# Kernel tuning notes

Measured on AMD Instinct MI355X. Metric: run time of the kernel, lower is better.

## Reference

```python
import jax, jax.numpy as jnp
import numpy as np

WIN = 7
N_HEADS = 12


def _swin_rel_pos_index(win_h, win_w):
    # standard Swin relative position index, flattened to (win_h*win_w)**2
    coords = np.stack(np.meshgrid(np.arange(win_h), np.arange(win_w), indexing='ij'))  # 2, Wh, Ww
    coords_flat = coords.reshape(2, -1)
    rel = coords_flat[:, :, None] - coords_flat[:, None, :]  # 2, N, N
    rel = rel.transpose(1, 2, 0).astype(np.int64)
    rel[:, :, 0] += win_h - 1
    rel[:, :, 1] += win_w - 1
    rel[:, :, 0] *= 2 * win_w - 1
    return rel.sum(-1).reshape(-1).astype(np.int32)  # (N*N,)


def setup_inputs() -> dict:
    key = jax.random.key(0)
    ks = jax.random.split(key, 8)
    B_, N, C = 4096, WIN * WIN, 384
    num_win = 64
    x = jax.random.normal(ks[0], (B_, N, C), dtype=jnp.float32)
    # 0 / -inf style additive mask (use -100 like Swin's masked_fill value)
    m = jax.random.uniform(ks[1], (num_win, N, N))
    mask = jnp.where(m < 0.5, 0.0, -100.0).astype(jnp.float32)
    qkv_w = jax.random.normal(ks[2], (3 * C, C), dtype=jnp.float32) * 0.02
    qkv_b = jax.random.normal(ks[3], (3 * C,), dtype=jnp.float32) * 0.02
    proj_w = jax.random.normal(ks[4], (C, C), dtype=jnp.float32) * 0.02
    proj_b = jax.random.normal(ks[5], (C,), dtype=jnp.float32) * 0.02
    bias_table = jax.random.normal(ks[6], ((2 * WIN - 1) ** 2, N_HEADS), dtype=jnp.float32) * 0.02
    rel_index = jnp.asarray(_swin_rel_pos_index(WIN, WIN))
    return {"x": x, "mask": mask, "qkv_w": qkv_w, "qkv_b": qkv_b,
            "proj_w": proj_w, "proj_b": proj_b, "bias_table": bias_table,
            "rel_index": rel_index}


def reference(x, mask, qkv_w, qkv_b, proj_w, proj_b, bias_table, rel_index):
    B_, N, C = x.shape
    H = N_HEADS
    hd = C // H
    scale = hd ** (-0.5)
    # qkv projection: (B_, N, 3C) -> (3, B_, H, N, hd)
    qkv = (jnp.einsum('bnc,oc->bno', x, qkv_w) + qkv_b)
    qkv = qkv.reshape(B_, N, 3, H, hd).transpose(2, 0, 3, 1, 4)
    q, k, v = qkv[0] * scale, qkv[1], qkv[2]
    attn = jnp.einsum('bhnd,bhmd->bhnm', q, k)  # (B_, H, N, N)
    # relative position bias gather: (N*N, H) -> (H, N, N)
    bias = bias_table[rel_index].reshape(N, N, H).transpose(2, 0, 1)
    attn = attn + bias[None]
    num_win = mask.shape[0]
    attn = attn.reshape(B_ // num_win, num_win, H, N, N) + mask[None, :, None]
    attn = attn.reshape(B_, H, N, N)
    attn = jax.nn.softmax(attn, axis=-1)
    out = jnp.einsum('bhnm,bhmd->bnhd', attn, v).reshape(B_, N, H * hd)
    out = jnp.einsum('bnc,oc->bno', out, proj_w) + proj_b
    return out
```

## Files before the change

### kernel.cpp

```cpp
#include <hip/hip_runtime.h>
#include <hip/hip_bf16.h>
#include <stdint.h>
#include <stddef.h>


typedef __attribute__((ext_vector_type(8))) __bf16 bf16x8;
typedef __attribute__((ext_vector_type(4))) float f32x4;
typedef __attribute__((ext_vector_type(4))) unsigned short u16x4;

typedef const unsigned int __attribute__((address_space(1)))* gptr_t;
typedef unsigned int __attribute__((address_space(3)))* lptr_t;

#define SCALE 0.17677669529663687f

__device__ __forceinline__ unsigned short f2bf(float f) {
  union { float f; unsigned int u; } c; c.f = f;
  unsigned int r = c.u + 0x7fffu + ((c.u >> 16) & 1u);
  return (unsigned short)(r >> 16);
}

__device__ __forceinline__ void gl_lds16(const void* g, void* s) {
  __builtin_amdgcn_global_load_lds((gptr_t)g, (lptr_t)s, 16, 0, 0);
}

__global__ __launch_bounds__(256) void convert_kernel(
    const float* __restrict__ x, unsigned short* __restrict__ xb, long nx4,
    const float* __restrict__ w1, unsigned short* __restrict__ w1b, long n14,
    const float* __restrict__ w2, unsigned short* __restrict__ w2b, long n24) {
  long stride = (long)gridDim.x * blockDim.x;
  long t0 = (long)blockIdx.x * blockDim.x + threadIdx.x;
  for (long i = t0; i < nx4; i += stride) {
    f32x4 v = ((const f32x4*)x)[i];
    u16x4 o;
#pragma unroll
    for (int j = 0; j < 4; ++j) o[j] = f2bf(v[j]);
    ((u16x4*)xb)[i] = o;
  }
  for (long i = t0; i < n14; i += stride) {
    f32x4 v = ((const f32x4*)w1)[i];
    u16x4 o;
#pragma unroll
    for (int j = 0; j < 4; ++j) o[j] = f2bf(v[j]);
    ((u16x4*)w1b)[i] = o;
  }
  for (long i = t0; i < n24; i += stride) {
    f32x4 v = ((const f32x4*)w2)[i];
    u16x4 o;
#pragma unroll
    for (int j = 0; j < 4; ++j) o[j] = f2bf(v[j]);
    ((u16x4*)w2b)[i] = o;
  }
}

__global__ __launch_bounds__(256) void cmb_kernel(
    const float* __restrict__ mask, const float* __restrict__ bias_table,
    const int* __restrict__ rel_index, float* __restrict__ cmb) {
  int idx = blockIdx.x * 256 + threadIdx.x;
  int j = idx & 63, i = (idx >> 6) & 63;
  int hw = idx >> 12;
  int h = hw % 12, w = hw / 12;
  float v = -1e30f;
  if (i < 49 && j < 49)
    v = bias_table[rel_index[i * 49 + j] * 12 + h] + mask[(w * 49 + i) * 49 + j];
  cmb[idx] = v;
}

template <int NBN, int KDIM, bool OUT_BF16>
__global__ __launch_bounds__(256) void gemm_nt(
    const unsigned short* __restrict__ A, const unsigned short* __restrict__ Bw,
    const float* __restrict__ bias, unsigned short* __restrict__ Cb,
    float* __restrict__ Cf, int Nn) {
  __shared__ __align__(16) unsigned short As[128 * 32];
  __shared__ __align__(16) unsigned short Bs[128 * 32];
  const int tid = threadIdx.x;
  const int w = tid >> 6, l = tid & 63, q = l >> 4, ln = l & 15;
  const int bm = blockIdx.x / NBN, bn = blockIdx.x % NBN;
  const unsigned short* Ab = A + (size_t)bm * 128 * KDIM;
  const unsigned short* Bb = Bw + (size_t)bn * 128 * KDIM;
  const int wm = w >> 1, wn = w & 1;
  const int lrow = l >> 2;
  const int lch = (l & 3) ^ ((l >> 3) & 3);
  f32x4 acc[4][4] = {};
  for (int k0 = 0; k0 < KDIM; k0 += 32) {
#pragma unroll
    for (int i = 0; i < 2; ++i) {
      int rowbase = (w * 2 + i) * 16;
      gl_lds16(Ab + (size_t)(rowbase + lrow) * KDIM + k0 + lch * 8,
               &As[rowbase * 32]);
      gl_lds16(Bb + (size_t)(rowbase + lrow) * KDIM + k0 + lch * 8,
               &Bs[rowbase * 32]);
    }
    __syncthreads();
    bf16x8 af[4], bf[4];
    const int ch = q ^ ((ln >> 1) & 3);
#pragma unroll
    for (int t = 0; t < 4; ++t) {
      af[t] = *(const bf16x8*)&As[(wm * 64 + t * 16 + ln) * 32 + ch * 8];
      bf[t] = *(const bf16x8*)&Bs[(wn * 64 + t * 16 + ln) * 32 + ch * 8];
    }
#pragma unroll
    for (int i = 0; i < 4; ++i)
#pragma unroll
      for (int j = 0; j < 4; ++j)
        acc[i][j] = __builtin_amdgcn_mfma_f32_16x16x32_bf16(af[i], bf[j],
                                                            acc[i][j], 0, 0, 0);
    __syncthreads();
  }
#pragma unroll
  for (int j = 0; j < 4; ++j) {
    int col = bn * 128 + wn * 64 + j * 16 + ln;
    float bv = bias[col];
#pragma unroll
    for (int i = 0; i < 4; ++i) {
      int row0 = bm * 128 + wm * 64 + i * 16 + q * 4;
#pragma unroll
      for (int r = 0; r < 4; ++r) {
        float v = acc[i][j][r] + bv;
        size_t off = (size_t)(row0 + r) * Nn + col;
        if constexpr (OUT_BF16) Cb[off] = f2bf(v);
        else Cf[off] = v;
      }
    }
  }
}

__global__ __launch_bounds__(256) void attn_kernel(
    const unsigned short* __restrict__ qkv, const float* __restrict__ cmb,
    unsigned short* __restrict__ aout) {
  __shared__ __align__(16) unsigned short Ps[4][64 * 80];
  const int tid = threadIdx.x;
  const int w = tid >> 6, l = tid & 63, q = l >> 4, ln = l & 15;
  const int pair = blockIdx.x * 4 + w;
  const int b = pair / 12, h = pair % 12;
  const int win = b & 63;
  const unsigned short* base = qkv + (size_t)b * 49 * 1152 + h * 32;
  bf16x8 qf[4], kf[4];
#pragma unroll
  for (int t = 0; t < 4; ++t) {
    int r = t * 16 + ln;
    int rr = (r < 49) ? r : 0;
    qf[t] = *(const bf16x8*)(base + (size_t)rr * 1152 + q * 8);
    kf[t] = *(const bf16x8*)(base + 384 + (size_t)rr * 1152 + q * 8);
  }
  f32x4 s[4][4] = {};
#pragma unroll
  for (int i = 0; i < 4; ++i)
#pragma unroll
    for (int j = 0; j < 4; ++j)
      s[i][j] = __builtin_amdgcn_mfma_f32_16x16x32_bf16(qf[i], kf[j], s[i][j],
                                                        0, 0, 0);
  const float* cb = cmb + ((size_t)win * 12 + h) * 4096;
#pragma unroll
  for (int mt = 0; mt < 4; ++mt) {
#pragma unroll
    for (int r = 0; r < 4; ++r) {
      int row = mt * 16 + q * 4 + r;
      float v[4];
#pragma unroll
      for (int nt = 0; nt < 4; ++nt)
        v[nt] = s[mt][nt][r] * SCALE + cb[row * 64 + nt * 16 + ln];
      float m = fmaxf(fmaxf(v[0], v[1]), fmaxf(v[2], v[3]));
#pragma unroll
      for (int off = 1; off < 16; off <<= 1)
        m = fmaxf(m, __shfl_xor(m, off, 64));
      float p[4], sum = 0.f;
#pragma unroll
      for (int nt = 0; nt < 4; ++nt) { p[nt] = __expf(v[nt] - m); sum += p[nt]; }
#pragma unroll
      for (int off = 1; off < 16; off <<= 1)
        sum += __shfl_xor(sum, off, 64);
      float inv = 1.0f / sum;
#pragma unroll
      for (int nt = 0; nt < 4; ++nt)
        Ps[w][row * 80 + nt * 16 + ln] = f2bf(p[nt] * inv);
    }
  }
  __syncthreads();
  const __bf16* vbase = (const __bf16*)(base + 768);
  bf16x8 vf[2][2];
#pragma unroll
  for (int nt = 0; nt < 2; ++nt)
#pragma unroll
    for (int kt = 0; kt < 2; ++kt) {
      bf16x8 tmp;
#pragma unroll
      for (int jj = 0; jj < 8; ++jj) {
        int j = kt * 32 + q * 8 + jj;
        int jc = (j < 49) ? j : 0;
        tmp[jj] = vbase[(size_t)jc * 1152 + nt * 16 + ln];
      }
      vf[nt][kt] = tmp;
    }
  f32x4 o[4][2] = {};
#pragma unroll
  for (int mt = 0; mt < 4; ++mt)
#pragma unroll
    for (int kt = 0; kt < 2; ++kt) {
      bf16x8 pf = *(const bf16x8*)&Ps[w][(mt * 16 + ln) * 80 + kt * 32 + q * 8];
#pragma unroll
      for (int nt = 0; nt < 2; ++nt)
        o[mt][nt] = __builtin_amdgcn_mfma_f32_16x16x32_bf16(pf, vf[nt][kt],
                                                            o[mt][nt], 0, 0, 0);
    }
#pragma unroll
  for (int mt = 0; mt < 4; ++mt)
#pragma unroll
    for (int r = 0; r < 4; ++r) {
      int n = mt * 16 + q * 4 + r;
      if (n < 49) {
#pragma unroll
        for (int nt = 0; nt < 2; ++nt)
          aout[((size_t)b * 49 + n) * 384 + h * 32 + nt * 16 + ln] =
              f2bf(o[mt][nt][r]);
      }
    }
}

extern "C" void kernel_launch(void* const* d_in, const int* in_sizes, int n_in,
                              void* d_out, int out_size, void* d_ws,
                              size_t ws_size, hipStream_t stream) {
  (void)in_sizes; (void)n_in; (void)out_size; (void)ws_size;
  const float* x          = (const float*)d_in[0];
  const float* mask       = (const float*)d_in[1];
  const float* qkv_w      = (const float*)d_in[2];
  const float* qkv_b      = (const float*)d_in[3];
  const float* proj_w     = (const float*)d_in[4];
  const float* proj_b     = (const float*)d_in[5];
  const float* bias_table = (const float*)d_in[6];
  const int*   rel_index  = (const int*)d_in[7];

  char* ws = (char*)d_ws;
  unsigned short* qkv  = (unsigned short*)ws;
  unsigned short* xb   = (unsigned short*)(ws + 462422016ull);
  unsigned short* aout = xb;
  unsigned short* wq   = (unsigned short*)(ws + 616562688ull);
  unsigned short* wp   = (unsigned short*)(ws + 617447424ull);
  float*          cmb  = (float*)(ws + 617742336ull);

  convert_kernel<<<2048, 256, 0, stream>>>(x, xb, 19267584L,
                                           qkv_w, wq, 110592L,
                                           proj_w, wp, 36864L);
  cmb_kernel<<<12288, 256, 0, stream>>>(mask, bias_table, rel_index, cmb);
  gemm_nt<9, 384, true><<<14112, 256, 0, stream>>>(xb, wq, qkv_b, qkv, nullptr,
                                                   1152);
  attn_kernel<<<12288, 256, 0, stream>>>(qkv, cmb, aout);
  gemm_nt<3, 384, false><<<4704, 256, 0, stream>>>(aout, wp, proj_b, nullptr,
                                                   (float*)d_out, 384);
}
```

Measured before the change: 1.262 ms.

## Double-buffer GEMM LDS loads, swizzle block order, stage bf16 epilogue through LDS

```diff
diff --git a/kernel.cpp b/kernel.cpp
--- a/kernel.cpp
+++ b/kernel.cpp
@@ -7,6 +7,7 @@
 typedef __attribute__((ext_vector_type(8))) __bf16 bf16x8;
 typedef __attribute__((ext_vector_type(4))) float f32x4;
 typedef __attribute__((ext_vector_type(4))) unsigned short u16x4;
+typedef __attribute__((ext_vector_type(8))) unsigned short u16x8;
 
 typedef const unsigned int __attribute__((address_space(1)))* gptr_t;
 typedef unsigned int __attribute__((address_space(3)))* lptr_t;
@@ -70,33 +71,56 @@
     const unsigned short* __restrict__ A, const unsigned short* __restrict__ Bw,
     const float* __restrict__ bias, unsigned short* __restrict__ Cb,
     float* __restrict__ Cf, int Nn) {
-  __shared__ __align__(16) unsigned short As[128 * 32];
-  __shared__ __align__(16) unsigned short Bs[128 * 32];
+  __shared__ __align__(16) unsigned short Sm[16384];
   const int tid = threadIdx.x;
   const int w = tid >> 6, l = tid & 63, q = l >> 4, ln = l & 15;
-  const int bm = blockIdx.x / NBN, bn = blockIdx.x % NBN;
+  const int cpx = gridDim.x >> 3;
+  const int swz = (blockIdx.x & 7) * cpx + (blockIdx.x >> 3);
+  const int bm = swz / NBN, bn = swz % NBN;
   const unsigned short* Ab = A + (size_t)bm * 128 * KDIM;
   const unsigned short* Bb = Bw + (size_t)bn * 128 * KDIM;
   const int wm = w >> 1, wn = w & 1;
   const int lrow = l >> 2;
   const int lch = (l & 3) ^ ((l >> 3) & 3);
-  f32x4 acc[4][4] = {};
-  for (int k0 = 0; k0 < KDIM; k0 += 32) {
+
+  float bv[4];
+#pragma unroll
+  for (int j = 0; j < 4; ++j) bv[j] = bias[bn * 128 + wn * 64 + j * 16 + ln];
+
+  auto stage = [&](int buf, int k0) {
+    unsigned short* as = Sm + buf * 4096;
+    unsigned short* bs = Sm + 8192 + buf * 4096;
 #pragma unroll
     for (int i = 0; i < 2; ++i) {
       int rowbase = (w * 2 + i) * 16;
       gl_lds16(Ab + (size_t)(rowbase + lrow) * KDIM + k0 + lch * 8,
-               &As[rowbase * 32]);
+               &as[rowbase * 32]);
       gl_lds16(Bb + (size_t)(rowbase + lrow) * KDIM + k0 + lch * 8,
-               &Bs[rowbase * 32]);
-    }
-    __syncthreads();
+               &bs[rowbase * 32]);
+    }
+  };
+
+  f32x4 acc[4][4] = {};
+  const int ch = q ^ ((ln >> 1) & 3);
+  constexpr int NIT = KDIM / 32;
+  stage(0, 0);
+  int cur = 0;
+#pragma unroll
+  for (int t = 0; t < NIT; ++t) {
+    if (t + 1 < NIT) {
+      stage(cur ^ 1, (t + 1) * 32);
+      asm volatile("s_waitcnt vmcnt(4)" ::: "memory");
+    } else {
+      asm volatile("s_waitcnt vmcnt(0)" ::: "memory");
+    }
+    __builtin_amdgcn_s_barrier();
+    const unsigned short* as = Sm + cur * 4096;
+    const unsigned short* bs = Sm + 8192 + cur * 4096;
     bf16x8 af[4], bf[4];
-    const int ch = q ^ ((ln >> 1) & 3);
-#pragma unroll
-    for (int t = 0; t < 4; ++t) {
-      af[t] = *(const bf16x8*)&As[(wm * 64 + t * 16 + ln) * 32 + ch * 8];
-      bf[t] = *(const bf16x8*)&Bs[(wn * 64 + t * 16 + ln) * 32 + ch * 8];
+#pragma unroll
+    for (int tt = 0; tt < 4; ++tt) {
+      af[tt] = *(const bf16x8*)&as[(wm * 64 + tt * 16 + ln) * 32 + ch * 8];
+      bf[tt] = *(const bf16x8*)&bs[(wn * 64 + tt * 16 + ln) * 32 + ch * 8];
     }
 #pragma unroll
     for (int i = 0; i < 4; ++i)
@@ -104,21 +128,52 @@
       for (int j = 0; j < 4; ++j)
         acc[i][j] = __builtin_amdgcn_mfma_f32_16x16x32_bf16(af[i], bf[j],
                                                             acc[i][j], 0, 0, 0);
-    __syncthreads();
-  }
-#pragma unroll
-  for (int j = 0; j < 4; ++j) {
-    int col = bn * 128 + wn * 64 + j * 16 + ln;
-    float bv = bias[col];
-#pragma unroll
-    for (int i = 0; i < 4; ++i) {
-      int row0 = bm * 128 + wm * 64 + i * 16 + q * 4;
-#pragma unroll
-      for (int r = 0; r < 4; ++r) {
-        float v = acc[i][j][r] + bv;
-        size_t off = (size_t)(row0 + r) * Nn + col;
-        if constexpr (OUT_BF16) Cb[off] = f2bf(v);
-        else Cf[off] = v;
+    asm volatile("s_waitcnt lgkmcnt(0)" ::: "memory");
+    __builtin_amdgcn_s_barrier();
+    cur ^= 1;
+  }
+
+  if constexpr (OUT_BF16) {
+    const int rr = tid >> 4, c8 = (tid & 15) * 8;
+    const size_t crow = (size_t)bm * 128;
+#pragma unroll
+    for (int half = 0; half < 2; ++half) {
+      if (wm == half) {
+#pragma unroll
+        for (int j = 0; j < 4; ++j) {
+          int col = wn * 64 + j * 16 + ln;
+#pragma unroll
+          for (int i = 0; i < 4; ++i) {
+            int r0 = i * 16 + q * 4;
+#pragma unroll
+            for (int r = 0; r < 4; ++r)
+              Sm[(r0 + r) * 132 + col] = f2bf(acc[i][j][r] + bv[j]);
+          }
+        }
+      }
+      __syncthreads();
+#pragma unroll
+      for (int p = 0; p < 4; ++p) {
+        int row = p * 16 + rr;
+        u16x4 v0 = *(const u16x4*)&Sm[row * 132 + c8];
+        u16x4 v1 = *(const u16x4*)&Sm[row * 132 + c8 + 4];
+        u16x8 v;
+#pragma unroll
+        for (int k = 0; k < 4; ++k) { v[k] = v0[k]; v[4 + k] = v1[k]; }
+        *(u16x8*)&Cb[(crow + half * 64 + row) * Nn + bn * 128 + c8] = v;
+      }
+      if (half == 0) __syncthreads();
+    }
+  } else {
+#pragma unroll
+    for (int j = 0; j < 4; ++j) {
+      int col = bn * 128 + wn * 64 + j * 16 + ln;
+#pragma unroll
+      for (int i = 0; i < 4; ++i) {
+        int row0 = bm * 128 + wm * 64 + i * 16 + q * 4;
+#pragma unroll
+        for (int r = 0; r < 4; ++r)
+          Cf[(size_t)(row0 + r) * Nn + col] = acc[i][j][r] + bv[j];
       }
     }
   }
```

Result: faster. 1.225 ms (-2.9%).
